# Performance work log

Measured on AMD Instinct MI355X. Metric: run time of the kernel, lower is better.

## Reference

```python
import jax, jax.numpy as jnp
import numpy as np

B, T, D = 256, 512, 256

def setup_inputs() -> dict:
    key = jax.random.key(0)
    k1, k2, k3, k4 = jax.random.split(key, 4)
    ip = jax.random.normal(k1, (B, T, D), dtype=jnp.float32)
    W = jax.random.normal(k2, (D, D), dtype=jnp.float32) * (1.0 / np.sqrt(D))
    b = jax.random.normal(k3, (D,), dtype=jnp.float32) * 0.05
    context = jax.random.normal(k4, (D, 1), dtype=jnp.float32) * 0.05
    return {"ip": ip, "W": W, "b": b, "context": context}

def reference(ip, W, b, context) -> jnp.ndarray:
    # linear -> tanh: [B, T, D]
    h = jnp.tanh(jnp.einsum("btd,ed->bte", ip, W) + b)
    # attention scores over words: [B, T]
    scores = jnp.einsum("btd,d->bt", h, context[:, 0])
    attn = jax.nn.softmax(scores, axis=1)
    # weighted sum over words -> sentence embeddings: [B, D]
    sent_embeds = jnp.einsum("bt,btd->bd", attn, ip)
    return sent_embeds
```

## Files before the change

kernel.cpp:

```cpp
#include <hip/hip_runtime.h>
#include <hip/hip_bf16.h>

#define NBATCH 256
#define NT 512
#define ND 256
#define NROWS (NBATCH * NT)
#define CHUNK 128
#define NCHUNK (NROWS / CHUNK)

typedef __attribute__((ext_vector_type(8))) short short8;
typedef __attribute__((ext_vector_type(4))) float floatx4;

__device__ __forceinline__ unsigned short f2bf(float x) {
    unsigned int u = __float_as_uint(x);
    u += 0x7FFFu + ((u >> 16) & 1u);
    return (unsigned short)(u >> 16);
}

__device__ __forceinline__ short8 cvt8(float4 lo, float4 hi) {
    short8 v;
    v[0] = (short)f2bf(lo.x); v[1] = (short)f2bf(lo.y);
    v[2] = (short)f2bf(lo.z); v[3] = (short)f2bf(lo.w);
    v[4] = (short)f2bf(hi.x); v[5] = (short)f2bf(hi.y);
    v[6] = (short)f2bf(hi.z); v[7] = (short)f2bf(hi.w);
    return v;
}

__global__ void __launch_bounds__(256) prep_kernel(
    const float* __restrict__ W, unsigned short* __restrict__ wf)
{
    int g  = blockIdx.x * 256 + threadIdx.x;
    int m  = g & 15, q = (g >> 4) & 3, s = (g >> 6) & 7, nb = g >> 9;
    const float* src = W + (nb * 16 + m) * ND + q * 8 + s * 32;
    float4 f0 = *(const float4*)src;
    float4 f1 = *(const float4*)(src + 4);
    *(short8*)(wf + (long)g * 8) = cvt8(f0, f1);
}

__global__ void __launch_bounds__(256, 4) fused_kernel(
    const float* __restrict__ ip,
    const unsigned short* __restrict__ wf,
    const float* __restrict__ bias,
    const float* __restrict__ ctx,
    float* __restrict__ gpart,
    float2* __restrict__ ml)
{
    __shared__ float score_s[CHUNK];
    __shared__ float w_s[CHUNK];
    __shared__ __align__(16) float partial[4][ND];

    const int tid  = threadIdx.x;
    const int lane = tid & 63;
    const int wv   = tid >> 6;
    const int m    = lane & 15;
    const int q    = lane >> 4;
    const long row0 = (long)blockIdx.x * CHUNK + wv * 32;

    short8 a0[8], a1[8];
    {
        const float* ar = ip + (row0 + m) * ND + q * 8;
        float4 raw[8];
#pragma unroll
        for (int g = 0; g < 2; ++g) {
#pragma unroll
            for (int i = 0; i < 4; ++i) {
                raw[2 * i]     = *(const float4*)(ar + (4 * g + i) * 32);
                raw[2 * i + 1] = *(const float4*)(ar + (4 * g + i) * 32 + 4);
            }
#pragma unroll
            for (int i = 0; i < 4; ++i)
                a0[4 * g + i] = cvt8(raw[2 * i], raw[2 * i + 1]);
        }
        const float* br = ar + 16 * ND;
#pragma unroll
        for (int g = 0; g < 2; ++g) {
#pragma unroll
            for (int i = 0; i < 4; ++i) {
                raw[2 * i]     = *(const float4*)(br + (4 * g + i) * 32);
                raw[2 * i + 1] = *(const float4*)(br + (4 * g + i) * 32 + 4);
            }
#pragma unroll
            for (int i = 0; i < 4; ++i)
                a1[4 * g + i] = cvt8(raw[2 * i], raw[2 * i + 1]);
        }
    }

    float sc0[4] = {0.f, 0.f, 0.f, 0.f};
    float sc1[4] = {0.f, 0.f, 0.f, 0.f};
    const short8* wch = (const short8*)wf;

#pragma unroll 1
    for (int nb = 0; nb < 16; ++nb) {
        const short8* wp = wch + nb * 512 + lane;
        short8 w[4];
        floatx4 acc0 = {0.f, 0.f, 0.f, 0.f};
        floatx4 acc1 = {0.f, 0.f, 0.f, 0.f};
#pragma unroll
        for (int s = 0; s < 4; ++s) w[s] = wp[s * 64];
#pragma unroll
        for (int s = 0; s < 4; ++s) {
            acc0 = __builtin_amdgcn_mfma_f32_16x16x32_bf16(a0[s], w[s], acc0, 0, 0, 0);
            acc1 = __builtin_amdgcn_mfma_f32_16x16x32_bf16(a1[s], w[s], acc1, 0, 0, 0);
        }
#pragma unroll
        for (int s = 0; s < 4; ++s) w[s] = wp[(s + 4) * 64];
#pragma unroll
        for (int s = 0; s < 4; ++s) {
            acc0 = __builtin_amdgcn_mfma_f32_16x16x32_bf16(a0[s + 4], w[s], acc0, 0, 0, 0);
            acc1 = __builtin_amdgcn_mfma_f32_16x16x32_bf16(a1[s + 4], w[s], acc1, 0, 0, 0);
        }
        const int e = nb * 16 + m;
        const float be  = bias[e];
        const float ce  = ctx[e];
        const float ce2 = ce + ce;
#pragma unroll
        for (int r = 0; r < 4; ++r) {
            float x0 = acc0[r] + be;
            float t0 = __builtin_amdgcn_rcpf(__expf(x0 + x0) + 1.f);
            sc0[r] = __builtin_fmaf(-ce2, t0, sc0[r] + ce);
            float x1 = acc1[r] + be;
            float t1 = __builtin_amdgcn_rcpf(__expf(x1 + x1) + 1.f);
            sc1[r] = __builtin_fmaf(-ce2, t1, sc1[r] + ce);
        }
    }

#pragma unroll
    for (int off = 8; off >= 1; off >>= 1) {
#pragma unroll
        for (int r = 0; r < 4; ++r) {
            sc0[r] += __shfl_xor(sc0[r], off, 64);
            sc1[r] += __shfl_xor(sc1[r], off, 64);
        }
    }
    if (m == 0) {
#pragma unroll
        for (int r = 0; r < 4; ++r) {
            score_s[wv * 32 + q * 4 + r]      = sc0[r];
            score_s[wv * 32 + 16 + q * 4 + r] = sc1[r];
        }
    }
    __syncthreads();

    float s0 = score_s[lane], s1 = score_s[64 + lane];
    float mx = fmaxf(s0, s1);
#pragma unroll
    for (int off = 32; off >= 1; off >>= 1) mx = fmaxf(mx, __shfl_xor(mx, off, 64));
    float e0v = __expf(s0 - mx), e1v = __expf(s1 - mx);
    float ls = e0v + e1v;
#pragma unroll
    for (int off = 32; off >= 1; off >>= 1) ls += __shfl_xor(ls, off, 64);
    if (wv == 0) { w_s[lane] = e0v; w_s[64 + lane] = e1v; }
    if (tid == 0) ml[blockIdx.x] = make_float2(mx, ls);
    __syncthreads();

    const float4* base = (const float4*)(ip + row0 * ND) + lane;
    float4 acc4 = {0.f, 0.f, 0.f, 0.f};
#pragma unroll 8
    for (int r = 0; r < 32; ++r) {
        const float wt = w_s[wv * 32 + r];
        const float4 v = base[(long)r * 64];
        acc4.x += wt * v.x; acc4.y += wt * v.y;
        acc4.z += wt * v.z; acc4.w += wt * v.w;
    }
    ((float4*)&partial[wv][0])[lane] = acc4;
    __syncthreads();
    {
        float r = partial[0][tid] + partial[1][tid]
                + partial[2][tid] + partial[3][tid];
        gpart[(long)blockIdx.x * ND + tid] = r;
    }
}

__global__ void __launch_bounds__(256) combine_kernel(
    const float4* __restrict__ gpart4,
    const float2* __restrict__ ml,
    float4* __restrict__ out4)
{
    const int b = blockIdx.x * 4 + (threadIdx.x >> 6);
    const int c = threadIdx.x & 63;
    const float2* mlb = ml + b * 4;
    float mk[4], lk[4];
#pragma unroll
    for (int k = 0; k < 4; ++k) { float2 p = mlb[k]; mk[k] = p.x; lk[k] = p.y; }
    float M = fmaxf(fmaxf(mk[0], mk[1]), fmaxf(mk[2], mk[3]));
    float L = 0.f, f[4];
#pragma unroll
    for (int k = 0; k < 4; ++k) { f[k] = __expf(mk[k] - M); L += f[k] * lk[k]; }
    float4 acc = {0.f, 0.f, 0.f, 0.f};
#pragma unroll
    for (int k = 0; k < 4; ++k) {
        float4 v = gpart4[(long)(b * 4 + k) * 64 + c];
        acc.x += f[k] * v.x; acc.y += f[k] * v.y;
        acc.z += f[k] * v.z; acc.w += f[k] * v.w;
    }
    float inv = 1.f / L;
    acc.x *= inv; acc.y *= inv; acc.z *= inv; acc.w *= inv;
    out4[(long)b * 64 + c] = acc;
}

extern "C" void kernel_launch(void* const* d_in, const int* in_sizes, int n_in,
                              void* d_out, int out_size, void* d_ws, size_t ws_size,
                              hipStream_t stream) {
    const float* ip   = (const float*)d_in[0];
    const float* W    = (const float*)d_in[1];
    const float* bias = (const float*)d_in[2];
    const float* ctx  = (const float*)d_in[3];

    unsigned short* wf = (unsigned short*)d_ws;
    float* gpart = (float*)((char*)d_ws + ND * ND * sizeof(unsigned short));
    float2* ml   = (float2*)((char*)gpart + (long)NCHUNK * ND * sizeof(float));

    prep_kernel<<<32, 256, 0, stream>>>(W, wf);
    fused_kernel<<<NCHUNK, 256, 0, stream>>>(ip, wf, bias, ctx, gpart, ml);
    combine_kernel<<<NBATCH / 4, 256, 0, stream>>>((const float4*)gpart, ml, (float4*)d_out);
}
```

Measured before the change: 238.3 us.

## Halve rows per wave and prefetch W fragments across loop iterations

Shrinks the block chunk from 128 to 64 rows, so each wave computes one 16-row MFMA tile instead of two. The combine kernel now merges 8 partial softmax chunks per batch. W fragments are double-buffered in registers, loading the next block's first half while the current one computes. This cuts register pressure and doubles the block count to improve latency hiding. In exchange each W fragment is reused only once per load, which doubles L2 traffic for W and adds more partial results to combine.

```diff
diff --git a/kernel.cpp b/kernel.cpp
--- a/kernel.cpp
+++ b/kernel.cpp
@@ -5,7 +5,7 @@
 #define NT 512
 #define ND 256
 #define NROWS (NBATCH * NT)
-#define CHUNK 128
+#define CHUNK 64
 #define NCHUNK (NROWS / CHUNK)
 
 typedef __attribute__((ext_vector_type(8))) short short8;
@@ -54,9 +54,9 @@
     const int wv   = tid >> 6;
     const int m    = lane & 15;
     const int q    = lane >> 4;
-    const long row0 = (long)blockIdx.x * CHUNK + wv * 32;
+    const long row0 = (long)blockIdx.x * CHUNK + wv * 16;
 
-    short8 a0[8], a1[8];
+    short8 a[8];
     {
         const float* ar = ip + (row0 + m) * ND + q * 8;
         float4 raw[8];
@@ -69,95 +69,75 @@
             }
 #pragma unroll
             for (int i = 0; i < 4; ++i)
-                a0[4 * g + i] = cvt8(raw[2 * i], raw[2 * i + 1]);
-        }
-        const float* br = ar + 16 * ND;
-#pragma unroll
-        for (int g = 0; g < 2; ++g) {
-#pragma unroll
-            for (int i = 0; i < 4; ++i) {
-                raw[2 * i]     = *(const float4*)(br + (4 * g + i) * 32);
-                raw[2 * i + 1] = *(const float4*)(br + (4 * g + i) * 32 + 4);
-            }
-#pragma unroll
-            for (int i = 0; i < 4; ++i)
-                a1[4 * g + i] = cvt8(raw[2 * i], raw[2 * i + 1]);
+                a[4 * g + i] = cvt8(raw[2 * i], raw[2 * i + 1]);
         }
     }
 
-    float sc0[4] = {0.f, 0.f, 0.f, 0.f};
-    float sc1[4] = {0.f, 0.f, 0.f, 0.f};
+    float sc[4] = {0.f, 0.f, 0.f, 0.f};
     const short8* wch = (const short8*)wf;
+
+    short8 w0[4], w1[4];
+#pragma unroll
+    for (int s = 0; s < 4; ++s) w0[s] = (wch + lane)[s * 64];
 
 #pragma unroll 1
     for (int nb = 0; nb < 16; ++nb) {
-        const short8* wp = wch + nb * 512 + lane;
-        short8 w[4];
-        floatx4 acc0 = {0.f, 0.f, 0.f, 0.f};
-        floatx4 acc1 = {0.f, 0.f, 0.f, 0.f};
+        const short8* wbase = wch + nb * 512 + lane;
 #pragma unroll
-        for (int s = 0; s < 4; ++s) w[s] = wp[s * 64];
+        for (int s = 0; s < 4; ++s) w1[s] = wbase[(s + 4) * 64];
+        const int e = nb * 16 + m;
+        const float be = bias[e];
+        const float ce = ctx[e];
+
+        floatx4 acc = {0.f, 0.f, 0.f, 0.f};
 #pragma unroll
-        for (int s = 0; s < 4; ++s) {
-            acc0 = __builtin_amdgcn_mfma_f32_16x16x32_bf16(a0[s], w[s], acc0, 0, 0, 0);
-            acc1 = __builtin_amdgcn_mfma_f32_16x16x32_bf16(a1[s], w[s], acc1, 0, 0, 0);
+        for (int s = 0; s < 4; ++s)
+            acc = __builtin_amdgcn_mfma_f32_16x16x32_bf16(a[s], w0[s], acc, 0, 0, 0);
+        if (nb < 15) {
+            const short8* wnext = wch + (nb + 1) * 512 + lane;
+#pragma unroll
+            for (int s = 0; s < 4; ++s) w0[s] = wnext[s * 64];
         }
 #pragma unroll
-        for (int s = 0; s < 4; ++s) w[s] = wp[(s + 4) * 64];
-#pragma unroll
-        for (int s = 0; s < 4; ++s) {
-            acc0 = __builtin_amdgcn_mfma_f32_16x16x32_bf16(a0[s + 4], w[s], acc0, 0, 0, 0);
-            acc1 = __builtin_amdgcn_mfma_f32_16x16x32_bf16(a1[s + 4], w[s], acc1, 0, 0, 0);
-        }
-        const int e = nb * 16 + m;
-        const float be  = bias[e];
-        const float ce  = ctx[e];
+        for (int s = 0; s < 4; ++s)
+            acc = __builtin_amdgcn_mfma_f32_16x16x32_bf16(a[s + 4], w1[s], acc, 0, 0, 0);
+
         const float ce2 = ce + ce;
 #pragma unroll
         for (int r = 0; r < 4; ++r) {
-            float x0 = acc0[r] + be;
-            float t0 = __builtin_amdgcn_rcpf(__expf(x0 + x0) + 1.f);
-            sc0[r] = __builtin_fmaf(-ce2, t0, sc0[r] + ce);
-            float x1 = acc1[r] + be;
-            float t1 = __builtin_amdgcn_rcpf(__expf(x1 + x1) + 1.f);
-            sc1[r] = __builtin_fmaf(-ce2, t1, sc1[r] + ce);
+            float x = acc[r] + be;
+            float t = __builtin_amdgcn_rcpf(__expf(x + x) + 1.f);
+            sc[r] = __builtin_fmaf(-ce2, t, sc[r] + ce);
         }
     }
 
 #pragma unroll
-    for (int off = 8; off >= 1; off >>= 1) {
+    for (int off = 8; off >= 1; off >>= 1)
 #pragma unroll
-        for (int r = 0; r < 4; ++r) {
-            sc0[r] += __shfl_xor(sc0[r], off, 64);
-            sc1[r] += __shfl_xor(sc1[r], off, 64);
-        }
-    }
-    if (m == 0) {
+        for (int r = 0; r < 4; ++r) sc[r] += __shfl_xor(sc[r], off, 64);
+    if (m == 0)
 #pragma unroll
-        for (int r = 0; r < 4; ++r) {
-            score_s[wv * 32 + q * 4 + r]      = sc0[r];
-            score_s[wv * 32 + 16 + q * 4 + r] = sc1[r];
-        }
-    }
+        for (int r = 0; r < 4; ++r) score_s[wv * 16 + q * 4 + r] = sc[r];
     __syncthreads();
 
-    float s0 = score_s[lane], s1 = score_s[64 + lane];
-    float mx = fmaxf(s0, s1);
+    float s0 = score_s[lane];
+    float mx = s0;
 #pragma unroll
     for (int off = 32; off >= 1; off >>= 1) mx = fmaxf(mx, __shfl_xor(mx, off, 64));
-    float e0v = __expf(s0 - mx), e1v = __expf(s1 - mx);
-    float ls = e0v + e1v;
+    float ev = __expf(s0 - mx);
+    float ls = ev;
 #pragma unroll
     for (int off = 32; off >= 1; off >>= 1) ls += __shfl_xor(ls, off, 64);
-    if (wv == 0) { w_s[lane] = e0v; w_s[64 + lane] = e1v; }
+    if (wv == 0) w_s[lane] = ev;
     if (tid == 0) ml[blockIdx.x] = make_float2(mx, ls);
     __syncthreads();
 
-    const float4* base = (const float4*)(ip + row0 * ND) + lane;
+    const int prow = wv * 16;
+    const float4* base = (const float4*)(ip + ((long)blockIdx.x * CHUNK + prow) * ND) + lane;
     float4 acc4 = {0.f, 0.f, 0.f, 0.f};
-#pragma unroll 8
-    for (int r = 0; r < 32; ++r) {
-        const float wt = w_s[wv * 32 + r];
+#pragma unroll
+    for (int r = 0; r < 16; ++r) {
+        const float wt = w_s[prow + r];
         const float4 v = base[(long)r * 64];
         acc4.x += wt * v.x; acc4.y += wt * v.y;
         acc4.z += wt * v.z; acc4.w += wt * v.w;
@@ -178,18 +158,20 @@
 {
     const int b = blockIdx.x * 4 + (threadIdx.x >> 6);
     const int c = threadIdx.x & 63;
-    const float2* mlb = ml + b * 4;
-    float mk[4], lk[4];
+    const float2* mlb = ml + b * 8;
+    float mk[8], lk[8];
 #pragma unroll
-    for (int k = 0; k < 4; ++k) { float2 p = mlb[k]; mk[k] = p.x; lk[k] = p.y; }
-    float M = fmaxf(fmaxf(mk[0], mk[1]), fmaxf(mk[2], mk[3]));
-    float L = 0.f, f[4];
+    for (int k = 0; k < 8; ++k) { float2 p = mlb[k]; mk[k] = p.x; lk[k] = p.y; }
+    float M = mk[0];
 #pragma unroll
-    for (int k = 0; k < 4; ++k) { f[k] = __expf(mk[k] - M); L += f[k] * lk[k]; }
+    for (int k = 1; k < 8; ++k) M = fmaxf(M, mk[k]);
+    float L = 0.f, f[8];
+#pragma unroll
+    for (int k = 0; k < 8; ++k) { f[k] = __expf(mk[k] - M); L += f[k] * lk[k]; }
     float4 acc = {0.f, 0.f, 0.f, 0.f};
 #pragma unroll
-    for (int k = 0; k < 4; ++k) {
-        float4 v = gpart4[(long)(b * 4 + k) * 64 + c];
+    for (int k = 0; k < 8; ++k) {
+        float4 v = gpart4[(long)(b * 8 + k) * 64 + c];
         acc.x += f[k] * v.x; acc.y += f[k] * v.y;
         acc.z += f[k] * v.z; acc.w += f[k] * v.w;
     }
```

Measured after the change: 229.1 us. 3.9% less time.

## Halve rows per block and split output features across wave pairs with W prefetch

Applied to the files above, without the earlier changes.

Rows per block drop from 128 to 64, and the four waves are split into two row groups times two halves of the output features, with partial scores summed in shared memory. The W fragment loop now double-buffers its loads, prefetching the next tile's first half during the MFMAs, and starts at a block-dependent offset to spread cache traffic. The combine kernel now merges eight chunks per batch instead of four. This doubles parallelism and hides W load latency, at the cost of more blocks, more partial outputs and the occupancy hint being removed.

```diff
diff --git a/kernel.cpp b/kernel.cpp
--- a/kernel.cpp
+++ b/kernel.cpp
@@ -5,7 +5,7 @@
 #define NT 512
 #define ND 256
 #define NROWS (NBATCH * NT)
-#define CHUNK 128
+#define CHUNK 64
 #define NCHUNK (NROWS / CHUNK)
 
 typedef __attribute__((ext_vector_type(8))) short short8;
@@ -37,7 +37,7 @@
     *(short8*)(wf + (long)g * 8) = cvt8(f0, f1);
 }
 
-__global__ void __launch_bounds__(256, 4) fused_kernel(
+__global__ void __launch_bounds__(256) fused_kernel(
     const float* __restrict__ ip,
     const unsigned short* __restrict__ wf,
     const float* __restrict__ bias,
@@ -45,16 +45,21 @@
     float* __restrict__ gpart,
     float2* __restrict__ ml)
 {
-    __shared__ float score_s[CHUNK];
+    __shared__ float score_p[2][CHUNK];
     __shared__ float w_s[CHUNK];
     __shared__ __align__(16) float partial[4][ND];
 
     const int tid  = threadIdx.x;
     const int lane = tid & 63;
     const int wv   = tid >> 6;
+    const int wr   = wv >> 1;
+    const int eh   = wv & 1;
     const int m    = lane & 15;
     const int q    = lane >> 4;
-    const long row0 = (long)blockIdx.x * CHUNK + wv * 32;
+    const long row0 = (long)blockIdx.x * CHUNK + wr * 32;
+    const int start = blockIdx.x & 7;
+
+    const short8* wch = (const short8*)wf;
 
     short8 a0[8], a1[8];
     {
@@ -87,31 +92,41 @@
 
     float sc0[4] = {0.f, 0.f, 0.f, 0.f};
     float sc1[4] = {0.f, 0.f, 0.f, 0.f};
-    const short8* wch = (const short8*)wf;
+
+    short8 w0[4], w1[4];
+#pragma unroll
+    for (int s = 0; s < 4; ++s)
+        w0[s] = (wch + (eh * 8 + start) * 512 + lane)[s * 64];
 
 #pragma unroll 1
-    for (int nb = 0; nb < 16; ++nb) {
-        const short8* wp = wch + nb * 512 + lane;
-        short8 w[4];
+    for (int i = 0; i < 8; ++i) {
+        const int t = (start + i) & 7;
+        const short8* wp = wch + (eh * 8 + t) * 512 + lane;
+#pragma unroll
+        for (int s = 0; s < 4; ++s) w1[s] = wp[(s + 4) * 64];
+        const int e = (eh * 8 + t) * 16 + m;
+        const float be = bias[e];
+        const float ce = ctx[e];
+
         floatx4 acc0 = {0.f, 0.f, 0.f, 0.f};
         floatx4 acc1 = {0.f, 0.f, 0.f, 0.f};
 #pragma unroll
-        for (int s = 0; s < 4; ++s) w[s] = wp[s * 64];
-#pragma unroll
         for (int s = 0; s < 4; ++s) {
-            acc0 = __builtin_amdgcn_mfma_f32_16x16x32_bf16(a0[s], w[s], acc0, 0, 0, 0);
-            acc1 = __builtin_amdgcn_mfma_f32_16x16x32_bf16(a1[s], w[s], acc1, 0, 0, 0);
-        }
-#pragma unroll
-        for (int s = 0; s < 4; ++s) w[s] = wp[(s + 4) * 64];
+            acc0 = __builtin_amdgcn_mfma_f32_16x16x32_bf16(a0[s], w0[s], acc0, 0, 0, 0);
+            acc1 = __builtin_amdgcn_mfma_f32_16x16x32_bf16(a1[s], w0[s], acc1, 0, 0, 0);
+        }
+        if (i < 7) {
+            const int tn = (start + i + 1) & 7;
+            const short8* wn = wch + (eh * 8 + tn) * 512 + lane;
+#pragma unroll
+            for (int s = 0; s < 4; ++s) w0[s] = wn[s * 64];
+        }
 #pragma unroll
         for (int s = 0; s < 4; ++s) {
-            acc0 = __builtin_amdgcn_mfma_f32_16x16x32_bf16(a0[s + 4], w[s], acc0, 0, 0, 0);
-            acc1 = __builtin_amdgcn_mfma_f32_16x16x32_bf16(a1[s + 4], w[s], acc1, 0, 0, 0);
-        }
-        const int e = nb * 16 + m;
-        const float be  = bias[e];
-        const float ce  = ctx[e];
+            acc0 = __builtin_amdgcn_mfma_f32_16x16x32_bf16(a0[s + 4], w1[s], acc0, 0, 0, 0);
+            acc1 = __builtin_amdgcn_mfma_f32_16x16x32_bf16(a1[s + 4], w1[s], acc1, 0, 0, 0);
+        }
+
         const float ce2 = ce + ce;
 #pragma unroll
         for (int r = 0; r < 4; ++r) {
@@ -135,29 +150,30 @@
     if (m == 0) {
 #pragma unroll
         for (int r = 0; r < 4; ++r) {
-            score_s[wv * 32 + q * 4 + r]      = sc0[r];
-            score_s[wv * 32 + 16 + q * 4 + r] = sc1[r];
+            score_p[eh][wr * 32 + q * 4 + r]      = sc0[r];
+            score_p[eh][wr * 32 + 16 + q * 4 + r] = sc1[r];
         }
     }
     __syncthreads();
 
-    float s0 = score_s[lane], s1 = score_s[64 + lane];
-    float mx = fmaxf(s0, s1);
+    float s0 = score_p[0][lane] + score_p[1][lane];
+    float mx = s0;
 #pragma unroll
     for (int off = 32; off >= 1; off >>= 1) mx = fmaxf(mx, __shfl_xor(mx, off, 64));
-    float e0v = __expf(s0 - mx), e1v = __expf(s1 - mx);
-    float ls = e0v + e1v;
+    float ev = __expf(s0 - mx);
+    float ls = ev;
 #pragma unroll
     for (int off = 32; off >= 1; off >>= 1) ls += __shfl_xor(ls, off, 64);
-    if (wv == 0) { w_s[lane] = e0v; w_s[64 + lane] = e1v; }
+    if (wv == 0) w_s[lane] = ev;
     if (tid == 0) ml[blockIdx.x] = make_float2(mx, ls);
     __syncthreads();
 
-    const float4* base = (const float4*)(ip + row0 * ND) + lane;
+    const int prow = wv * 16;
+    const float4* base = (const float4*)(ip + ((long)blockIdx.x * CHUNK + prow) * ND) + lane;
     float4 acc4 = {0.f, 0.f, 0.f, 0.f};
-#pragma unroll 8
-    for (int r = 0; r < 32; ++r) {
-        const float wt = w_s[wv * 32 + r];
+#pragma unroll
+    for (int r = 0; r < 16; ++r) {
+        const float wt = w_s[prow + r];
         const float4 v = base[(long)r * 64];
         acc4.x += wt * v.x; acc4.y += wt * v.y;
         acc4.z += wt * v.z; acc4.w += wt * v.w;
@@ -178,18 +194,20 @@
 {
     const int b = blockIdx.x * 4 + (threadIdx.x >> 6);
     const int c = threadIdx.x & 63;
-    const float2* mlb = ml + b * 4;
-    float mk[4], lk[4];
-#pragma unroll
-    for (int k = 0; k < 4; ++k) { float2 p = mlb[k]; mk[k] = p.x; lk[k] = p.y; }
-    float M = fmaxf(fmaxf(mk[0], mk[1]), fmaxf(mk[2], mk[3]));
-    float L = 0.f, f[4];
-#pragma unroll
-    for (int k = 0; k < 4; ++k) { f[k] = __expf(mk[k] - M); L += f[k] * lk[k]; }
+    const float2* mlb = ml + b * 8;
+    float mk[8], lk[8];
+#pragma unroll
+    for (int k = 0; k < 8; ++k) { float2 p = mlb[k]; mk[k] = p.x; lk[k] = p.y; }
+    float M = mk[0];
+#pragma unroll
+    for (int k = 1; k < 8; ++k) M = fmaxf(M, mk[k]);
+    float L = 0.f, f[8];
+#pragma unroll
+    for (int k = 0; k < 8; ++k) { f[k] = __expf(mk[k] - M); L += f[k] * lk[k]; }
     float4 acc = {0.f, 0.f, 0.f, 0.f};
 #pragma unroll
-    for (int k = 0; k < 4; ++k) {
-        float4 v = gpart4[(long)(b * 4 + k) * 64 + c];
+    for (int k = 0; k < 8; ++k) {
+        float4 v = gpart4[(long)(b * 8 + k) * 64 + c];
         acc.x += f[k] * v.x; acc.y += f[k] * v.y;
         acc.z += f[k] * v.z; acc.w += f[k] * v.w;
     }
```

New measurement: 223.6 us. -6.1%, faster.
